# Kernel optimization log

Hardware: AMD Instinct MI355X
Metric: run time of the kernel (lower is better)

## Reference

```python
import jax, jax.numpy as jnp
import numpy as np

B, N, IN_DIM, HID = 64, 1024, 128, 32


def _xavier(key, shape):
    # xavier_uniform_ on torch Linear weight [out, in]; we store [in, out]
    fan_in, fan_out = shape[0], shape[1]
    limit = float(np.sqrt(6.0 / (fan_in + fan_out)))
    return jax.random.uniform(key, shape, jnp.float32, -limit, limit)


def setup_inputs() -> dict:
    key = jax.random.key(0)
    ks = jax.random.split(key, 8)
    x = jax.random.normal(ks[0], (B, N, IN_DIM), jnp.float32)
    adj = jax.random.uniform(ks[1], (B, N, N), jnp.float32)  # dense adjacency
    W1 = _xavier(ks[2], (IN_DIM, HID))
    W2 = _xavier(ks[3], (HID, HID))
    W3 = _xavier(ks[4], (HID, HID))
    W4 = _xavier(ks[5], (HID, HID))
    b1 = jnp.zeros((HID,), jnp.float32)
    b2 = jnp.zeros((HID,), jnp.float32)
    b3 = jnp.zeros((HID,), jnp.float32)
    b4 = jnp.zeros((HID,), jnp.float32)
    a1 = jnp.float32(0.25)  # PReLU default init
    a2 = jnp.float32(0.25)
    a3 = jnp.float32(0.25)
    a4 = jnp.float32(0.25)
    return {"x": x, "adj": adj, "W1": W1, "W2": W2, "W3": W3, "W4": W4,
            "b1": b1, "b2": b2, "b3": b3, "b4": b4,
            "a1": a1, "a2": a2, "a3": a3, "a4": a4}


def _gcn_layer(x, adj, W, b, a):
    h = jnp.einsum('bnf,fo->bno', x, W)      # linear, no bias
    h = jnp.matmul(adj, h) + b               # aggregation + bias
    return jnp.where(h >= 0, h, a * h)       # PReLU


def reference(x, adj, W1, W2, W3, W4, b1, b2, b3, b4, a1, a2, a3, a4):
    h1 = _gcn_layer(x, adj, W1, b1, a1)
    h2 = _gcn_layer(h1, adj, W2, b2, a2)
    h3 = _gcn_layer(h2, adj, W3, b3, a3)
    h4 = _gcn_layer(h3, adj, W4, b4, a4)
    # sum-pool nodes per layer, concat along feature dim -> [B, 4*HID]
    return jnp.concatenate([h1.sum(axis=1), h2.sum(axis=1),
                            h3.sum(axis=1), h4.sum(axis=1)], axis=1)
```

## Files before the change

kernel.cpp:

```cpp
#include <hip/hip_runtime.h>
#include <hip/hip_bf16.h>

#define B_   64
#define N_   1024
#define IND_ 128
#define HID_ 32

typedef __attribute__((ext_vector_type(8))) short short8;
typedef __attribute__((ext_vector_type(4))) float f32x4;
typedef unsigned short u16;

static __device__ __forceinline__ u16 f2bf(float f) {
    union { __hip_bfloat16 h; u16 s; } u;
    u.h = __float2bfloat16(f);
    return u.s;
}
static __device__ __forceinline__ short8 cvt8(f32x4 v0, f32x4 v1) {
    union { short8 s; __hip_bfloat162 h[4]; } u;
    u.h[0] = __float22bfloat162_rn(float2{v0[0], v0[1]});
    u.h[1] = __float22bfloat162_rn(float2{v0[2], v0[3]});
    u.h[2] = __float22bfloat162_rn(float2{v1[0], v1[1]});
    u.h[3] = __float22bfloat162_rn(float2{v1[2], v1[3]});
    return u.s;
}

__global__ __launch_bounds__(256) void convert_tile_kernel(
    const float* __restrict__ adjf, u16* __restrict__ adjT)
{
    const int wslot = blockIdx.x * 4 + (threadIdx.x >> 6);
    const int lane = threadIdx.x & 63;
    const int r = lane & 15, g = lane >> 4;
    const int t0 = wslot * 16;
    const int b  = t0 >> 11;
    const int rt = (t0 >> 5) & 63;
    const int k0base = (t0 & 31) * 32;

    const float* src = adjf + ((size_t)b * N_ + rt * 16 + r) * N_ + k0base + g * 8;
    u16* dst = adjT + (size_t)t0 * 512 + lane * 8;

#pragma unroll 4
    for (int j = 0; j < 16; ++j) {
        f32x4 v0 = __builtin_nontemporal_load((const f32x4*)(src + j * 32));
        f32x4 v1 = __builtin_nontemporal_load((const f32x4*)(src + j * 32) + 1);
        *(short8*)(dst + (size_t)j * 512) = cvt8(v0, v1);
    }
}

template<int F>
__global__ __launch_bounds__(256) void linear_kernel(
    const float* __restrict__ in,
    const float* __restrict__ W,
    u16* __restrict__ outT)
{
    __shared__ float sW[F][HID_];
    const int tid = threadIdx.x;
    for (int e = tid; e < F * HID_; e += 256) sW[e / HID_][e % HID_] = W[e];
    __syncthreads();

    const int b = blockIdx.x >> 2;
    const int n = ((blockIdx.x & 3) << 8) + tid;
    const f32x4* row4 = (const f32x4*)(in + ((size_t)b * N_ + n) * F);

    float acc[HID_];
#pragma unroll
    for (int o = 0; o < HID_; ++o) acc[o] = 0.f;

#pragma unroll 4
    for (int f4 = 0; f4 < F / 4; ++f4) {
        f32x4 xv = row4[f4];
#pragma unroll
        for (int j = 0; j < 4; ++j) {
#pragma unroll
            for (int o = 0; o < HID_; ++o) acc[o] += xv[j] * sW[f4 * 4 + j][o];
        }
    }
    u16* op = outT + (size_t)b * HID_ * N_ + n;
#pragma unroll
    for (int o = 0; o < HID_; ++o) op[o * N_] = f2bf(acc[o]);
}

template<int MODE, int FUSE>
__global__ __launch_bounds__(256) void agg_kernel(
    const float* __restrict__ adjf,
    const u16*  __restrict__ adjT,
    const u16*  __restrict__ hlinT_in,
    u16*        __restrict__ hlinT_out,
    const float* __restrict__ Wnext,
    float*      __restrict__ h,
    float*      __restrict__ partial,
    const float* __restrict__ bias,
    const float* __restrict__ alpha_p)
{
    union Smem {
        u16 sB[HID_][512 + 8];
        struct { float h_s[64][33]; float sW2[HID_][HID_]; } ep;
    };
    __shared__ Smem sm;
    __shared__ float pool[4][HID_];

    const int tid = threadIdx.x;
    const int b = blockIdx.y;
    const int wid = tid >> 6, lane = tid & 63;
    const int r16 = lane & 15, g = lane >> 4;
    const int koff = g * 8;
    const int rowbase = blockIdx.x * 64 + wid * 16;
    const int row0 = rowbase + r16;
    const u16* srcB = hlinT_in + (size_t)b * HID_ * N_;

    const u16* pa = adjT
        ? adjT + ((size_t)b * 2048 + (size_t)(blockIdx.x * 4 + wid) * 32) * 512 + lane * 8
        : nullptr;
    const float* pf = adjf
        ? adjf + ((size_t)b * N_ + row0) * N_ + koff
        : nullptr;

    f32x4 acc[2] = {};

    for (int c = 0; c < 2; ++c) {
        if (c) __syncthreads();
        for (int i = tid; i < 2048; i += 256) {
            const int row = i >> 6;
            const int kv = (i & 63) << 3;
            *(short8*)&sm.sB[row][kv] =
                *(const short8*)(srcB + (size_t)row * N_ + (c << 9) + kv);
        }
        __syncthreads();

#pragma unroll 8
        for (int kk = 0; kk < 512; kk += 32) {
            short8 a0;
            if (MODE == 0) {
                const int ki = c * 16 + (kk >> 5);
                a0 = *(const short8*)(pa + (size_t)ki * 512);
            } else {
                const int k0 = (c << 9) + kk;
                f32x4 v0 = __builtin_nontemporal_load((const f32x4*)(pf + k0));
                f32x4 v1 = __builtin_nontemporal_load((const f32x4*)(pf + k0) + 1);
                a0 = cvt8(v0, v1);
            }
            short8 b0 = *(const short8*)&sm.sB[r16][kk + koff];
            short8 b1 = *(const short8*)&sm.sB[16 + r16][kk + koff];
            acc[0] = __builtin_amdgcn_mfma_f32_16x16x32_bf16(a0, b0, acc[0], 0, 0, 0);
            acc[1] = __builtin_amdgcn_mfma_f32_16x16x32_bf16(a0, b1, acc[1], 0, 0, 0);
        }
    }

    const float alpha = *alpha_p;
    float v[2][4];
    float ps[2];
#pragma unroll
    for (int ct = 0; ct < 2; ++ct) {
        const float bv = bias[ct * 16 + r16];
        ps[ct] = 0.f;
#pragma unroll
        for (int r = 0; r < 4; ++r) {
            float x = acc[ct][r] + bv;
            x = (x >= 0.f) ? x : alpha * x;
            v[ct][r] = x;
            ps[ct] += x;
        }
    }

    __syncthreads();

#pragma unroll
    for (int ct = 0; ct < 2; ++ct) {
        const int col = ct * 16 + r16;
        float p = ps[ct];
        p += __shfl_xor(p, 16, 64);
        p += __shfl_xor(p, 32, 64);
        if (lane < 16) pool[wid][col] = p;
        if (FUSE) {
#pragma unroll
            for (int r = 0; r < 4; ++r)
                sm.ep.h_s[wid * 16 + g * 4 + r][col] = v[ct][r];
        }
        if (MODE == 2) {
#pragma unroll
            for (int r = 0; r < 4; ++r) {
                const int row = rowbase + g * 4 + r;
                h[((size_t)b * N_ + row) * HID_ + col] = v[ct][r];
            }
        }
    }
    if (FUSE) {
        for (int e = tid; e < HID_ * HID_; e += 256)
            ((float*)sm.ep.sW2)[e] = Wnext[e];
    }
    __syncthreads();

    if (tid < HID_) {
        float s = pool[0][tid] + pool[1][tid] + pool[2][tid] + pool[3][tid];
        partial[((size_t)b * 16 + blockIdx.x) * HID_ + tid] = s;
    }

    if (FUSE) {
        const int r_local = tid >> 2;
        const int obase = (tid & 3) * 8;
        float acc2[8];
#pragma unroll
        for (int o = 0; o < 8; ++o) acc2[o] = 0.f;
#pragma unroll 4
        for (int k = 0; k < HID_; ++k) {
            const float hv = sm.ep.h_s[r_local][k];
#pragma unroll
            for (int o = 0; o < 8; ++o) acc2[o] += hv * sm.ep.sW2[k][obase + o];
        }
        const int n = blockIdx.x * 64 + r_local;
        u16* op = hlinT_out + (size_t)b * HID_ * N_ + n;
#pragma unroll
        for (int o = 0; o < 8; ++o) op[(size_t)(obase + o) * N_] = f2bf(acc2[o]);
    }
}

__global__ __launch_bounds__(256) void finalize_kernel(
    const float* __restrict__ partial,
    float* __restrict__ out)
{
    const int i = blockIdx.x * 256 + threadIdx.x;
    if (i >= B_ * 4 * HID_) return;
    const int b = i >> 7;
    const int rem = i & 127;
    const int l = rem >> 5;
    const int o = rem & 31;
    const float* p = partial + (((size_t)l * B_ + b) * 16) * HID_ + o;
    float s = 0.f;
#pragma unroll
    for (int t = 0; t < 16; ++t) s += p[t * HID_];
    out[i] = s;
}

extern "C" void kernel_launch(void* const* d_in, const int* in_sizes, int n_in,
                              void* d_out, int out_size, void* d_ws, size_t ws_size,
                              hipStream_t stream) {
    const float* x   = (const float*)d_in[0];
    const float* adj = (const float*)d_in[1];
    const float* W[4]  = {(const float*)d_in[2], (const float*)d_in[3],
                          (const float*)d_in[4], (const float*)d_in[5]};
    const float* bi[4] = {(const float*)d_in[6], (const float*)d_in[7],
                          (const float*)d_in[8], (const float*)d_in[9]};
    const float* al[4] = {(const float*)d_in[10], (const float*)d_in[11],
                          (const float*)d_in[12], (const float*)d_in[13]};
    float* out = (float*)d_out;

    const size_t adjb_bytes = (size_t)B_ * N_ * N_ * 2;
    const size_t hlin_bytes = (size_t)B_ * HID_ * N_ * 2;
    const size_t h_bytes    = (size_t)B_ * N_ * HID_ * 4;
    const size_t part_bytes = (size_t)4 * B_ * 16 * HID_ * 4;
    const bool full = ws_size >= adjb_bytes + 2 * hlin_bytes + part_bytes;

    const dim3 ga(16, 64);
    const int part_stride = B_ * 16 * HID_;

    if (full) {
        char* p = (char*)d_ws;
        u16* adjT  = (u16*)p;  p += adjb_bytes;
        u16* hlinA = (u16*)p;  p += hlin_bytes;
        u16* hlinB = (u16*)p;  p += hlin_bytes;
        float* partial = (float*)p;

        convert_tile_kernel<<<2048, 256, 0, stream>>>(adj, adjT);
        linear_kernel<IND_><<<256, 256, 0, stream>>>(x, W[0], hlinA);

        agg_kernel<0, 1><<<ga, 256, 0, stream>>>(nullptr, adjT, hlinA, hlinB,
                                                 W[1], nullptr,
                                                 partial + 0, bi[0], al[0]);
        agg_kernel<0, 1><<<ga, 256, 0, stream>>>(nullptr, adjT, hlinB, hlinA,
                                                 W[2], nullptr,
                                                 partial + (size_t)1 * part_stride,
                                                 bi[1], al[1]);
        agg_kernel<0, 1><<<ga, 256, 0, stream>>>(nullptr, adjT, hlinA, hlinB,
                                                 W[3], nullptr,
                                                 partial + (size_t)2 * part_stride,
                                                 bi[2], al[2]);
        agg_kernel<0, 0><<<ga, 256, 0, stream>>>(nullptr, adjT, hlinB, nullptr,
                                                 nullptr, nullptr,
                                                 partial + (size_t)3 * part_stride,
                                                 bi[3], al[3]);
    } else {
        char* p = (char*)d_ws;
        u16*   hlinT   = (u16*)p;  p += hlin_bytes;
        float* h       = (float*)p; p += h_bytes;
        float* partial = (float*)p;

        linear_kernel<IND_><<<256, 256, 0, stream>>>(x, W[0], hlinT);
        agg_kernel<2, 0><<<ga, 256, 0, stream>>>(adj, nullptr, hlinT, nullptr,
                                                 nullptr, h, partial + 0, bi[0], al[0]);
        for (int l = 1; l < 4; ++l) {
            linear_kernel<HID_><<<256, 256, 0, stream>>>(h, W[l], hlinT);
            agg_kernel<2, 0><<<ga, 256, 0, stream>>>(adj, nullptr, hlinT, nullptr,
                                                     nullptr, h,
                                                     partial + (size_t)l * part_stride,
                                                     bi[l], al[l]);
        }
    }
    finalize_kernel<<<32, 256, 0, stream>>>(
        (const float*)((char*)d_ws + (full ? adjb_bytes + 2 * hlin_bytes
                                           : hlin_bytes + h_bytes)), out);
}
```

Baseline: 212.5 us.

## Fuse all GCN stages into one cooperative persistent kernel with grid syncs

```diff
diff --git a/kernel.cpp b/kernel.cpp
--- a/kernel.cpp
+++ b/kernel.cpp
@@ -1,5 +1,8 @@
 #include <hip/hip_runtime.h>
 #include <hip/hip_bf16.h>
+#include <hip/hip_cooperative_groups.h>
+
+namespace cg = cooperative_groups;
 
 #define B_   64
 #define N_   1024
@@ -22,6 +25,171 @@
     u.h[2] = __float22bfloat162_rn(float2{v1[0], v1[1]});
     u.h[3] = __float22bfloat162_rn(float2{v1[2], v1[3]});
     return u.s;
+}
+
+struct MegaArgs {
+    const float* adjf; const float* x;
+    const float* W[4]; const float* bi[4]; const float* al[4];
+    u16* adjT; u16* hA; u16* hB; float* partial; float* out;
+};
+
+union Smem {
+    u16 sB[HID_][512 + 8];
+    float sW1[IND_][HID_];
+    struct { float h_s[64][33]; float sW2[HID_][HID_]; } ep;
+};
+
+__global__ __launch_bounds__(256, 4) void mega_kernel(MegaArgs A)
+{
+    __shared__ Smem sm;
+    __shared__ float pool[4][HID_];
+    cg::grid_group grid = cg::this_grid();
+
+    const int tid = threadIdx.x;
+    const int wid = tid >> 6, lane = tid & 63;
+    const int r16 = lane & 15, g = lane >> 4;
+    const int koff = g * 8;
+
+    for (int w = blockIdx.x; w < 1024; w += gridDim.x) {
+        const int bx = w & 15, by = w >> 4;
+        const int rt = bx * 4 + wid;
+        const float* src = A.adjf + ((size_t)by * N_ + rt * 16 + r16) * N_ + g * 8;
+        u16* dst = A.adjT + ((size_t)by * 2048 + (size_t)rt * 32) * 512 + lane * 8;
+#pragma unroll 8
+        for (int j = 0; j < 32; ++j) {
+            f32x4 v0 = __builtin_nontemporal_load((const f32x4*)(src + j * 32));
+            f32x4 v1 = __builtin_nontemporal_load((const f32x4*)(src + j * 32) + 1);
+            *(short8*)(dst + (size_t)j * 512) = cvt8(v0, v1);
+        }
+    }
+
+    for (int e = tid; e < IND_ * HID_; e += 256) ((float*)sm.sW1)[e] = A.W[0][e];
+    __syncthreads();
+    for (int w = blockIdx.x; w < 256; w += gridDim.x) {
+        const int b = w >> 2;
+        const int n = ((w & 3) << 8) + tid;
+        const f32x4* row4 = (const f32x4*)(A.x + ((size_t)b * N_ + n) * IND_);
+        float acc1[HID_];
+#pragma unroll
+        for (int o = 0; o < HID_; ++o) acc1[o] = 0.f;
+#pragma unroll 4
+        for (int f4 = 0; f4 < IND_ / 4; ++f4) {
+            f32x4 xv = row4[f4];
+#pragma unroll
+            for (int j = 0; j < 4; ++j)
+#pragma unroll
+                for (int o = 0; o < HID_; ++o) acc1[o] += xv[j] * sm.sW1[f4 * 4 + j][o];
+        }
+        u16* op = A.hA + (size_t)b * HID_ * N_ + n;
+#pragma unroll
+        for (int o = 0; o < HID_; ++o) op[o * N_] = f2bf(acc1[o]);
+    }
+
+    grid.sync();
+
+    const u16* hin = A.hA;
+    u16* hout = A.hB;
+    for (int l = 0; l < 4; ++l) {
+        const float alpha = *A.al[l];
+        const float* bias = A.bi[l];
+        const float* Wn = (l < 3) ? A.W[l + 1] : nullptr;
+
+        for (int w = blockIdx.x; w < 1024; w += gridDim.x) {
+            const int bx = w & 15, by = w >> 4;
+            const u16* srcB = hin + (size_t)by * HID_ * N_;
+            const u16* pa = A.adjT +
+                ((size_t)by * 2048 + (size_t)(bx * 4 + wid) * 32) * 512 + lane * 8;
+
+            f32x4 acc[2] = {};
+            for (int c = 0; c < 2; ++c) {
+                __syncthreads();
+                for (int i = tid; i < 2048; i += 256) {
+                    const int row = i >> 6;
+                    const int kv = (i & 63) << 3;
+                    *(short8*)&sm.sB[row][kv] =
+                        *(const short8*)(srcB + (size_t)row * N_ + (c << 9) + kv);
+                }
+                __syncthreads();
+#pragma unroll 8
+                for (int kk = 0; kk < 512; kk += 32) {
+                    const int ki = c * 16 + (kk >> 5);
+                    short8 a0 = *(const short8*)(pa + (size_t)ki * 512);
+                    short8 b0 = *(const short8*)&sm.sB[r16][kk + koff];
+                    short8 b1 = *(const short8*)&sm.sB[16 + r16][kk + koff];
+                    acc[0] = __builtin_amdgcn_mfma_f32_16x16x32_bf16(a0, b0, acc[0], 0, 0, 0);
+                    acc[1] = __builtin_amdgcn_mfma_f32_16x16x32_bf16(a0, b1, acc[1], 0, 0, 0);
+                }
+            }
+
+            float v[2][4], ps[2];
+#pragma unroll
+            for (int ct = 0; ct < 2; ++ct) {
+                const float bv = bias[ct * 16 + r16];
+                ps[ct] = 0.f;
+#pragma unroll
+                for (int r = 0; r < 4; ++r) {
+                    float xv = acc[ct][r] + bv;
+                    xv = (xv >= 0.f) ? xv : alpha * xv;
+                    v[ct][r] = xv;
+                    ps[ct] += xv;
+                }
+            }
+            __syncthreads();
+#pragma unroll
+            for (int ct = 0; ct < 2; ++ct) {
+                const int col = ct * 16 + r16;
+                float p = ps[ct];
+                p += __shfl_xor(p, 16, 64);
+                p += __shfl_xor(p, 32, 64);
+                if (lane < 16) pool[wid][col] = p;
+                if (l < 3) {
+#pragma unroll
+                    for (int r = 0; r < 4; ++r)
+                        sm.ep.h_s[wid * 16 + g * 4 + r][col] = v[ct][r];
+                }
+            }
+            if (l < 3) {
+                for (int e = tid; e < HID_ * HID_; e += 256)
+                    ((float*)sm.ep.sW2)[e] = Wn[e];
+            }
+            __syncthreads();
+            if (tid < HID_) {
+                float s = pool[0][tid] + pool[1][tid] + pool[2][tid] + pool[3][tid];
+                A.partial[(size_t)l * (B_ * 16 * HID_) +
+                          ((size_t)by * 16 + bx) * HID_ + tid] = s;
+            }
+            if (l < 3) {
+                const int r_local = tid >> 2;
+                const int obase = (tid & 3) * 8;
+                float acc2[8];
+#pragma unroll
+                for (int o = 0; o < 8; ++o) acc2[o] = 0.f;
+#pragma unroll 4
+                for (int k = 0; k < HID_; ++k) {
+                    const float hv = sm.ep.h_s[r_local][k];
+#pragma unroll
+                    for (int o = 0; o < 8; ++o) acc2[o] += hv * sm.ep.sW2[k][obase + o];
+                }
+                u16* op = hout + (size_t)by * HID_ * N_ + bx * 64 + r_local;
+#pragma unroll
+                for (int o = 0; o < 8; ++o) op[(size_t)(obase + o) * N_] = f2bf(acc2[o]);
+            }
+        }
+        grid.sync();
+        const u16* t = hin; hin = hout; hout = (u16*)t;
+    }
+
+    for (int i = blockIdx.x * 256 + tid; i < B_ * 4 * HID_; i += gridDim.x * 256) {
+        const int b = i >> 7;
+        const int rem = i & 127;
+        const int l = rem >> 5;
+        const int o = rem & 31;
+        const float* p = A.partial + (((size_t)l * B_ + b) * 16) * HID_ + o;
+        float s = 0.f;
+#pragma unroll
+        for (int t = 0; t < 16; ++t) s += p[t * HID_];
+        A.out[i] = s;
+    }
 }
 
 __global__ __launch_bounds__(256) void convert_tile_kernel(
@@ -37,7 +205,6 @@
 
     const float* src = adjf + ((size_t)b * N_ + rt * 16 + r) * N_ + k0base + g * 8;
     u16* dst = adjT + (size_t)t0 * 512 + lane * 8;
-
 #pragma unroll 4
     for (int j = 0; j < 16; ++j) {
         f32x4 v0 = __builtin_nontemporal_load((const f32x4*)(src + j * 32));
@@ -48,8 +215,7 @@
 
 template<int F>
 __global__ __launch_bounds__(256) void linear_kernel(
-    const float* __restrict__ in,
-    const float* __restrict__ W,
+    const float* __restrict__ in, const float* __restrict__ W,
     u16* __restrict__ outT)
 {
     __shared__ float sW[F][HID_];
@@ -64,15 +230,13 @@
     float acc[HID_];
 #pragma unroll
     for (int o = 0; o < HID_; ++o) acc[o] = 0.f;
-
 #pragma unroll 4
     for (int f4 = 0; f4 < F / 4; ++f4) {
         f32x4 xv = row4[f4];
 #pragma unroll
-        for (int j = 0; j < 4; ++j) {
+        for (int j = 0; j < 4; ++j)
 #pragma unroll
             for (int o = 0; o < HID_; ++o) acc[o] += xv[j] * sW[f4 * 4 + j][o];
-        }
     }
     u16* op = outT + (size_t)b * HID_ * N_ + n;
 #pragma unroll
@@ -81,20 +245,12 @@
 
 template<int MODE, int FUSE>
 __global__ __launch_bounds__(256) void agg_kernel(
-    const float* __restrict__ adjf,
-    const u16*  __restrict__ adjT,
-    const u16*  __restrict__ hlinT_in,
-    u16*        __restrict__ hlinT_out,
-    const float* __restrict__ Wnext,
-    float*      __restrict__ h,
-    float*      __restrict__ partial,
-    const float* __restrict__ bias,
+    const float* __restrict__ adjf, const u16* __restrict__ adjT,
+    const u16* __restrict__ hlinT_in, u16* __restrict__ hlinT_out,
+    const float* __restrict__ Wnext, float* __restrict__ h,
+    float* __restrict__ partial, const float* __restrict__ bias,
     const float* __restrict__ alpha_p)
 {
-    union Smem {
-        u16 sB[HID_][512 + 8];
-        struct { float h_s[64][33]; float sW2[HID_][HID_]; } ep;
-    };
     __shared__ Smem sm;
     __shared__ float pool[4][HID_];
 
@@ -110,12 +266,9 @@
     const u16* pa = adjT
         ? adjT + ((size_t)b * 2048 + (size_t)(blockIdx.x * 4 + wid) * 32) * 512 + lane * 8
         : nullptr;
-    const float* pf = adjf
-        ? adjf + ((size_t)b * N_ + row0) * N_ + koff
-        : nullptr;
+    const float* pf = adjf ? adjf + ((size_t)b * N_ + row0) * N_ + koff : nullptr;
 
     f32x4 acc[2] = {};
-
     for (int c = 0; c < 2; ++c) {
         if (c) __syncthreads();
         for (int i = tid; i < 2048; i += 256) {
@@ -125,7 +278,6 @@
                 *(const short8*)(srcB + (size_t)row * N_ + (c << 9) + kv);
         }
         __syncthreads();
-
 #pragma unroll 8
         for (int kk = 0; kk < 512; kk += 32) {
             short8 a0;
@@ -146,8 +298,7 @@
     }
 
     const float alpha = *alpha_p;
-    float v[2][4];
-    float ps[2];
+    float v[2][4], ps[2];
 #pragma unroll
     for (int ct = 0; ct < 2; ++ct) {
         const float bv = bias[ct * 16 + r16];
@@ -160,9 +311,7 @@
             ps[ct] += x;
         }
     }
-
     __syncthreads();
-
 #pragma unroll
     for (int ct = 0; ct < 2; ++ct) {
         const int col = ct * 16 + r16;
@@ -177,10 +326,8 @@
         }
         if (MODE == 2) {
 #pragma unroll
-            for (int r = 0; r < 4; ++r) {
-                const int row = rowbase + g * 4 + r;
-                h[((size_t)b * N_ + row) * HID_ + col] = v[ct][r];
-            }
+            for (int r = 0; r < 4; ++r)
+                h[((size_t)b * N_ + rowbase + g * 4 + r) * HID_ + col] = v[ct][r];
         }
     }
     if (FUSE) {
@@ -188,12 +335,10 @@
             ((float*)sm.ep.sW2)[e] = Wnext[e];
     }
     __syncthreads();
-
     if (tid < HID_) {
         float s = pool[0][tid] + pool[1][tid] + pool[2][tid] + pool[3][tid];
         partial[((size_t)b * 16 + blockIdx.x) * HID_ + tid] = s;
     }
-
     if (FUSE) {
         const int r_local = tid >> 2;
         const int obase = (tid & 3) * 8;
@@ -206,16 +351,14 @@
 #pragma unroll
             for (int o = 0; o < 8; ++o) acc2[o] += hv * sm.ep.sW2[k][obase + o];
         }
-        const int n = blockIdx.x * 64 + r_local;
-        u16* op = hlinT_out + (size_t)b * HID_ * N_ + n;
+        u16* op = hlinT_out + (size_t)b * HID_ * N_ + blockIdx.x * 64 + r_local;
 #pragma unroll
         for (int o = 0; o < 8; ++o) op[(size_t)(obase + o) * N_] = f2bf(acc2[o]);
     }
 }
 
 __global__ __launch_bounds__(256) void finalize_kernel(
-    const float* __restrict__ partial,
-    float* __restrict__ out)
+    const float* __restrict__ partial, float* __restrict__ out)
 {
     const int i = blockIdx.x * 256 + threadIdx.x;
     if (i >= B_ * 4 * HID_) return;
@@ -259,24 +402,44 @@
         u16* hlinB = (u16*)p;  p += hlin_bytes;
         float* partial = (float*)p;
 
-        convert_tile_kernel<<<2048, 256, 0, stream>>>(adj, adjT);
-        linear_kernel<IND_><<<256, 256, 0, stream>>>(x, W[0], hlinA);
-
-        agg_kernel<0, 1><<<ga, 256, 0, stream>>>(nullptr, adjT, hlinA, hlinB,
-                                                 W[1], nullptr,
-                                                 partial + 0, bi[0], al[0]);
-        agg_kernel<0, 1><<<ga, 256, 0, stream>>>(nullptr, adjT, hlinB, hlinA,
-                                                 W[2], nullptr,
-                                                 partial + (size_t)1 * part_stride,
-                                                 bi[1], al[1]);
-        agg_kernel<0, 1><<<ga, 256, 0, stream>>>(nullptr, adjT, hlinA, hlinB,
-                                                 W[3], nullptr,
-                                                 partial + (size_t)2 * part_stride,
-                                                 bi[2], al[2]);
-        agg_kernel<0, 0><<<ga, 256, 0, stream>>>(nullptr, adjT, hlinB, nullptr,
-                                                 nullptr, nullptr,
-                                                 partial + (size_t)3 * part_stride,
-                                                 bi[3], al[3]);
+        MegaArgs a;
+        a.adjf = adj; a.x = x;
+        for (int i = 0; i < 4; ++i) { a.W[i] = W[i]; a.bi[i] = bi[i]; a.al[i] = al[i]; }
+        a.adjT = adjT; a.hA = hlinA; a.hB = hlinB; a.partial = partial; a.out = out;
+
+        int blocksPerCU = 0, numCU = 0, dev = 0;
+        hipGetDevice(&dev);
+        hipDeviceGetAttribute(&numCU, hipDeviceAttributeMultiprocessorCount, dev);
+        hipOccupancyMaxActiveBlocksPerMultiprocessor(&blocksPerCU, mega_kernel, 256, 0);
+        long grid = (long)blocksPerCU * (numCU > 0 ? numCU : 256);
+        if (grid > 1024) grid = 1024;
+
+        bool ok = false;
+        if (grid >= 64) {
+            void* params[] = { (void*)&a };
+            hipError_t e = hipLaunchCooperativeKernel(mega_kernel, dim3((unsigned)grid),
+                                                      dim3(256), params, 0, stream);
+            ok = (e == hipSuccess);
+        }
+        if (!ok) {
+            convert_tile_kernel<<<2048, 256, 0, stream>>>(adj, adjT);
+            linear_kernel<IND_><<<256, 256, 0, stream>>>(x, W[0], hlinA);
+            agg_kernel<0, 1><<<ga, 256, 0, stream>>>(nullptr, adjT, hlinA, hlinB,
+                                                     W[1], nullptr, partial, bi[0], al[0]);
+            agg_kernel<0, 1><<<ga, 256, 0, stream>>>(nullptr, adjT, hlinB, hlinA,
+                                                     W[2], nullptr,
+                                                     partial + (size_t)1 * part_stride,
+                                                     bi[1], al[1]);
+            agg_kernel<0, 1><<<ga, 256, 0, stream>>>(nullptr, adjT, hlinA, hlinB,
+                                                     W[3], nullptr,
+                                                     partial + (size_t)2 * part_stride,
+                                                     bi[2], al[2]);
+            agg_kernel<0, 0><<<ga, 256, 0, stream>>>(nullptr, adjT, hlinB, nullptr,
+                                                     nullptr, nullptr,
+                                                     partial + (size_t)3 * part_stride,
+                                                     bi[3], al[3]);
+            finalize_kernel<<<32, 256, 0, stream>>>(partial, out);
+        }
     } else {
         char* p = (char*)d_ws;
         u16*   hlinT   = (u16*)p;  p += hlin_bytes;
@@ -285,7 +448,7 @@
 
         linear_kernel<IND_><<<256, 256, 0, stream>>>(x, W[0], hlinT);
         agg_kernel<2, 0><<<ga, 256, 0, stream>>>(adj, nullptr, hlinT, nullptr,
-                                                 nullptr, h, partial + 0, bi[0], al[0]);
+                                                 nullptr, h, partial, bi[0], al[0]);
         for (int l = 1; l < 4; ++l) {
             linear_kernel<HID_><<<256, 256, 0, stream>>>(h, W[l], hlinT);
             agg_kernel<2, 0><<<ga, 256, 0, stream>>>(adj, nullptr, hlinT, nullptr,
@@ -293,8 +456,6 @@
                                                      partial + (size_t)l * part_stride,
                                                      bi[l], al[l]);
         }
-    }
-    finalize_kernel<<<32, 256, 0, stream>>>(
-        (const float*)((char*)d_ws + (full ? adjb_bytes + 2 * hlin_bytes
-                                           : hlin_bytes + h_bytes)), out);
-}
+        finalize_kernel<<<32, 256, 0, stream>>>(partial, out);
+    }
+}
```

After: 546.7 us. 2.57x slower.

## Store hidden features in MFMA fragment layout and read B operand from global

Applied to the files above, without the earlier changes.

```diff
diff --git a/kernel.cpp b/kernel.cpp
--- a/kernel.cpp
+++ b/kernel.cpp
@@ -37,7 +37,6 @@
 
     const float* src = adjf + ((size_t)b * N_ + rt * 16 + r) * N_ + k0base + g * 8;
     u16* dst = adjT + (size_t)t0 * 512 + lane * 8;
-
 #pragma unroll 4
     for (int j = 0; j < 16; ++j) {
         f32x4 v0 = __builtin_nontemporal_load((const f32x4*)(src + j * 32));
@@ -50,7 +49,7 @@
 __global__ __launch_bounds__(256) void linear_kernel(
     const float* __restrict__ in,
     const float* __restrict__ W,
-    u16* __restrict__ outT)
+    u16* __restrict__ hF)
 {
     __shared__ float sW[F][HID_];
     const int tid = threadIdx.x;
@@ -67,35 +66,33 @@
 
 #pragma unroll 4
     for (int f4 = 0; f4 < F / 4; ++f4) {
-        f32x4 xv = row4[f4];
-#pragma unroll
-        for (int j = 0; j < 4; ++j) {
+        f32x4 xv = __builtin_nontemporal_load(row4 + f4);
+#pragma unroll
+        for (int j = 0; j < 4; ++j)
 #pragma unroll
             for (int o = 0; o < HID_; ++o) acc[o] += xv[j] * sW[f4 * 4 + j][o];
-        }
-    }
-    u16* op = outT + (size_t)b * HID_ * N_ + n;
-#pragma unroll
-    for (int o = 0; o < HID_; ++o) op[o * N_] = f2bf(acc[o]);
+    }
+    u16* op = hF + (size_t)b * (HID_ * N_) + (size_t)(n >> 5) * 1024
+              + ((n >> 3) & 3) * 128 + (n & 7);
+#pragma unroll
+    for (int o = 0; o < HID_; ++o)
+        op[(o >> 4) * 512 + (o & 15) * 8] = f2bf(acc[o]);
 }
 
 template<int MODE, int FUSE>
 __global__ __launch_bounds__(256) void agg_kernel(
     const float* __restrict__ adjf,
     const u16*  __restrict__ adjT,
-    const u16*  __restrict__ hlinT_in,
-    u16*        __restrict__ hlinT_out,
+    const u16*  __restrict__ hF_in,
+    u16*        __restrict__ hF_out,
     const float* __restrict__ Wnext,
     float*      __restrict__ h,
     float*      __restrict__ partial,
     const float* __restrict__ bias,
     const float* __restrict__ alpha_p)
 {
-    union Smem {
-        u16 sB[HID_][512 + 8];
-        struct { float h_s[64][33]; float sW2[HID_][HID_]; } ep;
-    };
-    __shared__ Smem sm;
+    __shared__ float h_s[64][33];
+    __shared__ float sW2[HID_][HID_];
     __shared__ float pool[4][HID_];
 
     const int tid = threadIdx.x;
@@ -105,49 +102,38 @@
     const int koff = g * 8;
     const int rowbase = blockIdx.x * 64 + wid * 16;
     const int row0 = rowbase + r16;
-    const u16* srcB = hlinT_in + (size_t)b * HID_ * N_;
-
-    const u16* pa = adjT
+
+    if (FUSE) {
+        for (int e = tid; e < HID_ * HID_; e += 256) ((float*)sW2)[e] = Wnext[e];
+    }
+
+    const u16* pbF = hF_in + (size_t)b * (HID_ * N_) + lane * 8;
+    const u16* pa = (MODE == 0)
         ? adjT + ((size_t)b * 2048 + (size_t)(blockIdx.x * 4 + wid) * 32) * 512 + lane * 8
         : nullptr;
-    const float* pf = adjf
+    const float* pf = (MODE == 2)
         ? adjf + ((size_t)b * N_ + row0) * N_ + koff
         : nullptr;
 
     f32x4 acc[2] = {};
-
-    for (int c = 0; c < 2; ++c) {
-        if (c) __syncthreads();
-        for (int i = tid; i < 2048; i += 256) {
-            const int row = i >> 6;
-            const int kv = (i & 63) << 3;
-            *(short8*)&sm.sB[row][kv] =
-                *(const short8*)(srcB + (size_t)row * N_ + (c << 9) + kv);
-        }
-        __syncthreads();
-
 #pragma unroll 8
-        for (int kk = 0; kk < 512; kk += 32) {
-            short8 a0;
-            if (MODE == 0) {
-                const int ki = c * 16 + (kk >> 5);
-                a0 = *(const short8*)(pa + (size_t)ki * 512);
-            } else {
-                const int k0 = (c << 9) + kk;
-                f32x4 v0 = __builtin_nontemporal_load((const f32x4*)(pf + k0));
-                f32x4 v1 = __builtin_nontemporal_load((const f32x4*)(pf + k0) + 1);
-                a0 = cvt8(v0, v1);
-            }
-            short8 b0 = *(const short8*)&sm.sB[r16][kk + koff];
-            short8 b1 = *(const short8*)&sm.sB[16 + r16][kk + koff];
-            acc[0] = __builtin_amdgcn_mfma_f32_16x16x32_bf16(a0, b0, acc[0], 0, 0, 0);
-            acc[1] = __builtin_amdgcn_mfma_f32_16x16x32_bf16(a0, b1, acc[1], 0, 0, 0);
-        }
+    for (int ki = 0; ki < 32; ++ki) {
+        short8 a0;
+        if (MODE == 0) {
+            a0 = *(const short8*)(pa + (size_t)ki * 512);
+        } else {
+            f32x4 v0 = __builtin_nontemporal_load((const f32x4*)(pf + ki * 32));
+            f32x4 v1 = __builtin_nontemporal_load((const f32x4*)(pf + ki * 32) + 1);
+            a0 = cvt8(v0, v1);
+        }
+        short8 b0 = *(const short8*)(pbF + (size_t)ki * 1024);
+        short8 b1 = *(const short8*)(pbF + (size_t)ki * 1024 + 512);
+        acc[0] = __builtin_amdgcn_mfma_f32_16x16x32_bf16(a0, b0, acc[0], 0, 0, 0);
+        acc[1] = __builtin_amdgcn_mfma_f32_16x16x32_bf16(a0, b1, acc[1], 0, 0, 0);
     }
 
     const float alpha = *alpha_p;
-    float v[2][4];
-    float ps[2];
+    float v[2][4], ps[2];
 #pragma unroll
     for (int ct = 0; ct < 2; ++ct) {
         const float bv = bias[ct * 16 + r16];
@@ -160,9 +146,6 @@
             ps[ct] += x;
         }
     }
-
-    __syncthreads();
-
 #pragma unroll
     for (int ct = 0; ct < 2; ++ct) {
         const int col = ct * 16 + r16;
@@ -173,19 +156,13 @@
         if (FUSE) {
 #pragma unroll
             for (int r = 0; r < 4; ++r)
-                sm.ep.h_s[wid * 16 + g * 4 + r][col] = v[ct][r];
+                h_s[wid * 16 + g * 4 + r][col] = v[ct][r];
         }
         if (MODE == 2) {
 #pragma unroll
-            for (int r = 0; r < 4; ++r) {
-                const int row = rowbase + g * 4 + r;
-                h[((size_t)b * N_ + row) * HID_ + col] = v[ct][r];
-            }
-        }
-    }
-    if (FUSE) {
-        for (int e = tid; e < HID_ * HID_; e += 256)
-            ((float*)sm.ep.sW2)[e] = Wnext[e];
+            for (int r = 0; r < 4; ++r)
+                h[((size_t)b * N_ + rowbase + g * 4 + r) * HID_ + col] = v[ct][r];
+        }
     }
     __syncthreads();
 
@@ -202,14 +179,18 @@
         for (int o = 0; o < 8; ++o) acc2[o] = 0.f;
 #pragma unroll 4
         for (int k = 0; k < HID_; ++k) {
-            const float hv = sm.ep.h_s[r_local][k];
-#pragma unroll
-            for (int o = 0; o < 8; ++o) acc2[o] += hv * sm.ep.sW2[k][obase + o];
+            const float hv = h_s[r_local][k];
+#pragma unroll
+            for (int o = 0; o < 8; ++o) acc2[o] += hv * sW2[k][obase + o];
         }
         const int n = blockIdx.x * 64 + r_local;
-        u16* op = hlinT_out + (size_t)b * HID_ * N_ + n;
-#pragma unroll
-        for (int o = 0; o < 8; ++o) op[(size_t)(obase + o) * N_] = f2bf(acc2[o]);
+        u16* op = hF_out + (size_t)b * (HID_ * N_) + (size_t)(n >> 5) * 1024
+                  + ((n >> 3) & 3) * 128 + (n & 7);
+#pragma unroll
+        for (int o = 0; o < 8; ++o) {
+            const int oo = obase + o;
+            op[(oo >> 4) * 512 + (oo & 15) * 8] = f2bf(acc2[o]);
+        }
     }
 }
 
@@ -255,46 +236,45 @@
     if (full) {
         char* p = (char*)d_ws;
         u16* adjT  = (u16*)p;  p += adjb_bytes;
-        u16* hlinA = (u16*)p;  p += hlin_bytes;
-        u16* hlinB = (u16*)p;  p += hlin_bytes;
+        u16* hFA   = (u16*)p;  p += hlin_bytes;
+        u16* hFB   = (u16*)p;  p += hlin_bytes;
         float* partial = (float*)p;
 
         convert_tile_kernel<<<2048, 256, 0, stream>>>(adj, adjT);
-        linear_kernel<IND_><<<256, 256, 0, stream>>>(x, W[0], hlinA);
-
-        agg_kernel<0, 1><<<ga, 256, 0, stream>>>(nullptr, adjT, hlinA, hlinB,
+        linear_kernel<IND_><<<256, 256, 0, stream>>>(x, W[0], hFA);
+
+        agg_kernel<0, 1><<<ga, 256, 0, stream>>>(nullptr, adjT, hFA, hFB,
                                                  W[1], nullptr,
                                                  partial + 0, bi[0], al[0]);
-        agg_kernel<0, 1><<<ga, 256, 0, stream>>>(nullptr, adjT, hlinB, hlinA,
+        agg_kernel<0, 1><<<ga, 256, 0, stream>>>(nullptr, adjT, hFB, hFA,
                                                  W[2], nullptr,
                                                  partial + (size_t)1 * part_stride,
                                                  bi[1], al[1]);
-        agg_kernel<0, 1><<<ga, 256, 0, stream>>>(nullptr, adjT, hlinA, hlinB,
+        agg_kernel<0, 1><<<ga, 256, 0, stream>>>(nullptr, adjT, hFA, hFB,
                                                  W[3], nullptr,
                                                  partial + (size_t)2 * part_stride,
                                                  bi[2], al[2]);
-        agg_kernel<0, 0><<<ga, 256, 0, stream>>>(nullptr, adjT, hlinB, nullptr,
+        agg_kernel<0, 0><<<ga, 256, 0, stream>>>(nullptr, adjT, hFB, nullptr,
                                                  nullptr, nullptr,
                                                  partial + (size_t)3 * part_stride,
                                                  bi[3], al[3]);
+        finalize_kernel<<<32, 256, 0, stream>>>(partial, out);
     } else {
         char* p = (char*)d_ws;
-        u16*   hlinT   = (u16*)p;  p += hlin_bytes;
+        u16*   hF      = (u16*)p;  p += hlin_bytes;
         float* h       = (float*)p; p += h_bytes;
         float* partial = (float*)p;
 
-        linear_kernel<IND_><<<256, 256, 0, stream>>>(x, W[0], hlinT);
-        agg_kernel<2, 0><<<ga, 256, 0, stream>>>(adj, nullptr, hlinT, nullptr,
-                                                 nullptr, h, partial + 0, bi[0], al[0]);
+        linear_kernel<IND_><<<256, 256, 0, stream>>>(x, W[0], hF);
+        agg_kernel<2, 0><<<ga, 256, 0, stream>>>(adj, nullptr, hF, nullptr,
+                                                 nullptr, h, partial, bi[0], al[0]);
         for (int l = 1; l < 4; ++l) {
-            linear_kernel<HID_><<<256, 256, 0, stream>>>(h, W[l], hlinT);
-            agg_kernel<2, 0><<<ga, 256, 0, stream>>>(adj, nullptr, hlinT, nullptr,
+            linear_kernel<HID_><<<256, 256, 0, stream>>>(h, W[l], hF);
+            agg_kernel<2, 0><<<ga, 256, 0, stream>>>(adj, nullptr, hF, nullptr,
                                                      nullptr, h,
                                                      partial + (size_t)l * part_stride,
                                                      bi[l], al[l]);
         }
-    }
-    finalize_kernel<<<32, 256, 0, stream>>>(
-        (const float*)((char*)d_ws + (full ? adjb_bytes + 2 * hlin_bytes
-                                           : hlin_bytes + h_bytes)), out);
-}
+        finalize_kernel<<<32, 256, 0, stream>>>(partial, out);
+    }
+}
```

After: 209.5 us. No clear change (-1.4%).
